# Performance work log

Hardware: AMD Instinct MI355X
Metric: run time of the kernel (lower is better)

The kernel has to match this reference:

```python
import jax, jax.numpy as jnp
import numpy as np

DEP_NUM, HEAD_NUM, BSZ, DIM, REL = 96, 96, 16, 512, 128


def setup_inputs() -> dict:
    key = jax.random.key(0)
    k1, k2, k3, k4 = jax.random.split(key, 4)
    outs = jax.random.normal(k1, (DEP_NUM, BSZ, DIM), dtype=jnp.float32)
    graph_state = jax.random.normal(k2, (HEAD_NUM, BSZ, DIM), dtype=jnp.float32)
    # nn.init.normal_(std=0.02) for both weights, zero biases
    Wt = 0.02 * jax.random.normal(k3, (DIM, 2 * DIM), dtype=jnp.float32)
    bt = jnp.zeros((DIM,), dtype=jnp.float32)
    Wp = 0.02 * jax.random.normal(k4, (REL, DIM), dtype=jnp.float32)
    bp = jnp.zeros((REL,), dtype=jnp.float32)
    return {"outs": outs, "graph_state": graph_state, "Wt": Wt, "bt": bt, "Wp": Wp, "bp": bp}


def reference(outs, graph_state, Wt, bt, Wp, bp):
    # outs: [dep, b, D], graph_state: [head, b, D]
    # Linear(cat(dep, head)) == dep @ Wt[:, :D].T + head @ Wt[:, D:].T + bt
    D = outs.shape[-1]
    dep_proj = jnp.einsum('dbi,ei->dbe', outs, Wt[:, :D])           # [dep, b, D]
    head_proj = jnp.einsum('hbi,ei->hbe', graph_state, Wt[:, D:])   # [head, b, D]
    # broadcast-sum to pairwise: [dep, b, head, D]
    h = jax.nn.relu(dep_proj[:, :, None, :] + jnp.swapaxes(head_proj, 0, 1)[None] + bt)
    # dropout: identity in eval mode
    scores = jnp.einsum('dbhe,re->dbhr', h, Wp) + bp                # [dep, b, head, REL]
    nil = jnp.zeros(scores.shape[:-1] + (1,), dtype=scores.dtype)
    scores = jnp.concatenate([nil, scores], axis=-1)                # [dep, b, head, REL+1]
    return jax.nn.log_softmax(scores, axis=-1)
```

## Files before the change

### kernel.cpp

```cpp
#include <hip/hip_runtime.h>
#include <math.h>

#define DEP   96
#define HEADS 96
#define BSZ   16
#define DIM   512
#define REL   128
#define RELP  129

typedef __attribute__((ext_vector_type(8))) _Float16  half8;
typedef __attribute__((ext_vector_type(2))) __fp16    fp16x2;
typedef __attribute__((ext_vector_type(4))) float     floatx4;

__device__ __forceinline__ unsigned short f2h(float x) {
    union { _Float16 h; unsigned short u; } c;
    c.h = (_Float16)x;
    return c.u;
}
__device__ __forceinline__ unsigned pk_f2h(float a, float b) {
    union { fp16x2 h; unsigned u; } c;
    c.h = __builtin_amdgcn_cvt_pkrtz(a, b);
    return c.u;
}
__device__ __forceinline__ unsigned pk_add_h2(unsigned a, unsigned b) {
    unsigned r; asm("v_pk_add_f16 %0, %1, %2" : "=v"(r) : "v"(a), "v"(b)); return r;
}
__device__ __forceinline__ unsigned pk_max_h2(unsigned a, unsigned b) {
    unsigned r; asm("v_pk_max_f16 %0, %1, %2" : "=v"(r) : "v"(a), "v"(b)); return r;
}

#define PSS 72

__global__ __launch_bounds__(256) void proj_kernel(
    const float* __restrict__ outs, const float* __restrict__ graph,
    const float* __restrict__ Wt, const float* __restrict__ bt,
    const float* __restrict__ Wp,
    float* __restrict__ P1, unsigned short* __restrict__ P2H,
    unsigned short* __restrict__ WpH)
{
    {
        const int fb = (blockIdx.z * gridDim.y + blockIdx.y) * gridDim.x + blockIdx.x;
        if (fb < 32) {
            const int c = fb * 256 + (int)threadIdx.x;
            float4 a = *(const float4*)(Wp + (size_t)c * 8);
            float4 b = *(const float4*)(Wp + (size_t)c * 8 + 4);
            uint4 o;
            o.x = pk_f2h(a.x, a.y); o.y = pk_f2h(a.z, a.w);
            o.z = pk_f2h(b.x, b.y); o.w = pk_f2h(b.z, b.w);
            *(uint4*)(WpH + (size_t)c * 8) = o;
        }
    }

    const int z = blockIdx.z;
    const float* A = z ? graph : outs;
    const int off  = z ? DIM : 0;
    const int row0 = blockIdx.y * 32;
    const int col0 = blockIdx.x * 64;

    __shared__ __align__(16) unsigned short As[32 * PSS];
    __shared__ __align__(16) unsigned short Ws[64 * PSS];

    const int tid  = threadIdx.x;
    const int lane = tid & 63;
    const int wv   = tid >> 6;
    const int ln15 = lane & 15;
    const int quad = lane >> 4;
    const int mh   = wv & 1;
    const int nh   = wv >> 1;

    floatx4 acc[2];
    acc[0] = (floatx4){0.f,0.f,0.f,0.f};
    acc[1] = (floatx4){0.f,0.f,0.f,0.f};

    for (int kt = 0; kt < DIM; kt += 64) {
        {
            const int r  = tid >> 3;
            const int e8 = (tid & 7) * 8;
            const float* p = A + (size_t)(row0 + r) * DIM + kt + e8;
            float4 va = *(const float4*)p;
            float4 vb = *(const float4*)(p + 4);
            uint4 o;
            o.x = pk_f2h(va.x, va.y); o.y = pk_f2h(va.z, va.w);
            o.z = pk_f2h(vb.x, vb.y); o.w = pk_f2h(vb.z, vb.w);
            *(uint4*)&As[r * PSS + e8] = o;
        }
        #pragma unroll
        for (int q = 0; q < 2; ++q) {
            const int slot = q*256 + tid;
            const int r  = slot >> 3;
            const int e8 = (slot & 7) * 8;
            const float* p = Wt + (size_t)(col0 + r) * (2*DIM) + off + kt + e8;
            float4 va = *(const float4*)p;
            float4 vb = *(const float4*)(p + 4);
            uint4 o;
            o.x = pk_f2h(va.x, va.y); o.y = pk_f2h(va.z, va.w);
            o.z = pk_f2h(vb.x, vb.y); o.w = pk_f2h(vb.z, vb.w);
            *(uint4*)&Ws[r * PSS + e8] = o;
        }
        __syncthreads();
        #pragma unroll
        for (int ks = 0; ks < 64; ks += 32) {
            half8 af = *(const half8*)&As[(mh*16 + ln15) * PSS + ks + quad*8];
            #pragma unroll
            for (int nt = 0; nt < 2; ++nt) {
                half8 bf8 = *(const half8*)&Ws[(nh*32 + nt*16 + ln15) * PSS + ks + quad*8];
                acc[nt] = __builtin_amdgcn_mfma_f32_16x16x32_f16(af, bf8, acc[nt], 0, 0, 0);
            }
        }
        __syncthreads();
    }

    #pragma unroll
    for (int nt = 0; nt < 2; ++nt) {
        #pragma unroll
        for (int reg = 0; reg < 4; ++reg) {
            const int m = row0 + mh*16 + quad*4 + reg;
            const int n = col0 + nh*32 + nt*16 + ln15;
            float v = acc[nt][reg];
            if (!z) P1[(size_t)m * DIM + n] = v + bt[n];
            else    P2H[(size_t)m * DIM + n] = f2h(v);
        }
    }
}

#define HSS 72
#define WSS 72

__global__ __launch_bounds__(256, 4) void fused_kernel(
    const float* __restrict__ P1, const unsigned short* __restrict__ P2H,
    const unsigned short* __restrict__ WpH, const float* __restrict__ bp,
    float* __restrict__ out)
{
    const int db = blockIdx.x;
    const int b  = db & 15;

    __shared__ __align__(16) char arena[96*HSS*2 + 128*WSS*2];
    unsigned short* hs = (unsigned short*)arena;
    unsigned short* ws = (unsigned short*)(arena + 96*HSS*2);
    float* outb = (float*)arena;
    float* pmx  = (float*)(arena + 24768);
    float* pl   = pmx + 192;
    float* lseS = pl + 192;

    const int tid  = threadIdx.x;
    const int lane = tid & 63;
    const int wv   = tid >> 6;
    const int ln15 = lane & 15;
    const int quad = lane >> 4;
    const int mh   = wv & 1;
    const int nh   = wv >> 1;
    const int e8   = (tid & 7) * 8;

    const float* drow = P1 + (size_t)db * DIM;

    floatx4 acc[3][4];
    #pragma unroll
    for (int i = 0; i < 3; ++i)
        #pragma unroll
        for (int j = 0; j < 4; ++j) acc[i][j] = (floatx4){0.f,0.f,0.f,0.f};

    for (int kt = 0; kt < DIM; kt += 64) {
        float4 d0 = *(const float4*)(drow + kt + e8);
        float4 d1 = *(const float4*)(drow + kt + e8 + 4);
        uint4 dv;
        dv.x = pk_f2h(d0.x, d0.y); dv.y = pk_f2h(d0.z, d0.w);
        dv.z = pk_f2h(d1.x, d1.y); dv.w = pk_f2h(d1.z, d1.w);

        #pragma unroll
        for (int q = 0; q < 3; ++q) {
            const int h = (q*256 + tid) >> 3;
            uint4 pv = *(const uint4*)(P2H + ((size_t)h * BSZ + b) * DIM + kt + e8);
            uint4 o;
            o.x = pk_max_h2(pk_add_h2(pv.x, dv.x), 0u);
            o.y = pk_max_h2(pk_add_h2(pv.y, dv.y), 0u);
            o.z = pk_max_h2(pk_add_h2(pv.z, dv.z), 0u);
            o.w = pk_max_h2(pk_add_h2(pv.w, dv.w), 0u);
            *(uint4*)&hs[h * HSS + e8] = o;
        }
        #pragma unroll
        for (int q = 0; q < 4; ++q) {
            const int r = (q*256 + tid) >> 3;
            *(uint4*)&ws[r * WSS + e8] =
                *(const uint4*)(WpH + (size_t)r * DIM + kt + e8);
        }
        __syncthreads();

        #pragma unroll
        for (int ks = 0; ks < 64; ks += 32) {
            half8 af[3], bf[4];
            #pragma unroll
            for (int mt = 0; mt < 3; ++mt)
                af[mt] = *(const half8*)&hs[(mh*48 + mt*16 + ln15) * HSS + ks + quad*8];
            #pragma unroll
            for (int nt = 0; nt < 4; ++nt)
                bf[nt] = *(const half8*)&ws[(nh*64 + nt*16 + ln15) * WSS + ks + quad*8];
            #pragma unroll
            for (int nt = 0; nt < 4; ++nt)
                #pragma unroll
                for (int mt = 0; mt < 3; ++mt)
                    acc[mt][nt] = __builtin_amdgcn_mfma_f32_16x16x32_f16(
                        af[mt], bf[nt], acc[mt][nt], 0, 0, 0);
        }
        __syncthreads();
    }

    float bpv[4];
    #pragma unroll
    for (int nt = 0; nt < 4; ++nt) bpv[nt] = bp[nh*64 + nt*16 + ln15];

    #pragma unroll
    for (int mt = 0; mt < 3; ++mt) {
        #pragma unroll
        for (int reg = 0; reg < 4; ++reg) {
            const int m = mh*48 + mt*16 + quad*4 + reg;
            float s[4];
            #pragma unroll
            for (int nt = 0; nt < 4; ++nt) s[nt] = acc[mt][nt][reg] + bpv[nt];
            float mx = fmaxf(fmaxf(s[0], s[1]), fmaxf(s[2], s[3]));
            #pragma unroll
            for (int msk = 1; msk < 16; msk <<= 1) mx = fmaxf(mx, __shfl_xor(mx, msk));
            float l = 0.f;
            #pragma unroll
            for (int nt = 0; nt < 4; ++nt) l += __expf(s[nt] - mx);
            #pragma unroll
            for (int msk = 1; msk < 16; msk <<= 1) l += __shfl_xor(l, msk);
            if (ln15 == 0) { pmx[m*2 + nh] = mx; pl[m*2 + nh] = l; }
        }
    }
    __syncthreads();

    if (tid < 96) {
        const float mx0 = pmx[tid*2], mx1 = pmx[tid*2 + 1];
        const float MX = fmaxf(fmaxf(mx0, mx1), 0.f);
        const float L  = pl[tid*2] * __expf(mx0 - MX) + pl[tid*2 + 1] * __expf(mx1 - MX)
                       + __expf(-MX);
        lseS[tid] = MX + __logf(L);
    }
    __syncthreads();

    #pragma unroll
    for (int g = 0; g < 2; ++g) {
        if (mh == g) {
            #pragma unroll
            for (int mt = 0; mt < 3; ++mt) {
                #pragma unroll
                for (int reg = 0; reg < 4; ++reg) {
                    const int lrow = mt*16 + quad*4 + reg;
                    const float lse = lseS[g*48 + lrow];
                    #pragma unroll
                    for (int nt = 0; nt < 4; ++nt)
                        outb[lrow*RELP + 1 + nh*64 + nt*16 + ln15] =
                            acc[mt][nt][reg] + bpv[nt] - lse;
                    if (nh == 0 && ln15 == 0) outb[lrow*RELP] = -lse;
                }
            }
        }
        __syncthreads();
        float4* gout = (float4*)(out + (size_t)db * (HEADS*RELP) + g * (48*RELP));
        const float4* lsrc = (const float4*)outb;
        for (int j = tid; j < 1548; j += 256)
            gout[j] = lsrc[j];
        __syncthreads();
    }
}

extern "C" void kernel_launch(void* const* d_in, const int* in_sizes, int n_in,
                              void* d_out, int out_size, void* d_ws, size_t ws_size,
                              hipStream_t stream) {
    const float* outs  = (const float*)d_in[0];
    const float* graph = (const float*)d_in[1];
    const float* Wt    = (const float*)d_in[2];
    const float* bt    = (const float*)d_in[3];
    const float* Wp    = (const float*)d_in[4];
    const float* bp    = (const float*)d_in[5];
    float* out = (float*)d_out;

    float* P1           = (float*)d_ws;
    unsigned short* P2H = (unsigned short*)(P1 + 786432);
    unsigned short* WpH = P2H + 786432;

    proj_kernel<<<dim3(DIM/64, (DEP*BSZ)/32, 2), 256, 0, stream>>>(
        outs, graph, Wt, bt, Wp, P1, P2H, WpH);
    fused_kernel<<<DEP*BSZ, 256, 0, stream>>>(P1, P2H, WpH, bp, out);
}
```

Measured before the change: 160.0 us.

## Shrink LDS footprint with 32-wide K tiles and direct output stores

Halves the K tile from 64 to 32, shrinking the shared-memory arena from about 31KB to about 19KB. The dep row is converted to fp16 once into LDS instead of being reloaded from global memory every K step. The LDS-staged coalesced float4 output write is dropped in favour of direct scattered global stores from the MFMA registers. The aim is more resident blocks per CU and fewer redundant loads, at the cost of twice as many barriers in the K loop and less coalesced output writes.

```diff
diff --git a/kernel.cpp b/kernel.cpp
--- a/kernel.cpp
+++ b/kernel.cpp
@@ -123,8 +123,7 @@
     }
 }
 
-#define HSS 72
-#define WSS 72
+#define HS2 40
 
 __global__ __launch_bounds__(256, 4) void fused_kernel(
     const float* __restrict__ P1, const unsigned short* __restrict__ P2H,
@@ -134,11 +133,11 @@
     const int db = blockIdx.x;
     const int b  = db & 15;
 
-    __shared__ __align__(16) char arena[96*HSS*2 + 128*WSS*2];
-    unsigned short* hs = (unsigned short*)arena;
-    unsigned short* ws = (unsigned short*)(arena + 96*HSS*2);
-    float* outb = (float*)arena;
-    float* pmx  = (float*)(arena + 24768);
+    __shared__ __align__(16) char arena[18944];
+    unsigned short* hs    = (unsigned short*)arena;
+    unsigned short* ws    = (unsigned short*)(arena + 7680);
+    unsigned short* drowH = (unsigned short*)(arena + 17920);
+    float* pmx  = (float*)arena;
     float* pl   = pmx + 192;
     float* lseS = pl + 192;
 
@@ -149,9 +148,14 @@
     const int quad = lane >> 4;
     const int mh   = wv & 1;
     const int nh   = wv >> 1;
-    const int e8   = (tid & 7) * 8;
-
-    const float* drow = P1 + (size_t)db * DIM;
+    const int e8   = (tid & 3) * 8;
+    const int r0   = tid >> 2;
+
+    {
+        float2 v = *(const float2*)(P1 + (size_t)db * DIM + tid*2);
+        *(unsigned*)&drowH[tid*2] = pk_f2h(v.x, v.y);
+    }
+    __syncthreads();
 
     floatx4 acc[3][4];
     #pragma unroll
@@ -159,41 +163,44 @@
         #pragma unroll
         for (int j = 0; j < 4; ++j) acc[i][j] = (floatx4){0.f,0.f,0.f,0.f};
 
-    for (int kt = 0; kt < DIM; kt += 64) {
-        float4 d0 = *(const float4*)(drow + kt + e8);
-        float4 d1 = *(const float4*)(drow + kt + e8 + 4);
-        uint4 dv;
-        dv.x = pk_f2h(d0.x, d0.y); dv.y = pk_f2h(d0.z, d0.w);
-        dv.z = pk_f2h(d1.x, d1.y); dv.w = pk_f2h(d1.z, d1.w);
-
-        #pragma unroll
-        for (int q = 0; q < 3; ++q) {
-            const int h = (q*256 + tid) >> 3;
+    for (int kt = 0; kt < DIM; kt += 32) {
+        uint4 dv = *(const uint4*)&drowH[kt + e8];
+        {
+            const int h = r0;
             uint4 pv = *(const uint4*)(P2H + ((size_t)h * BSZ + b) * DIM + kt + e8);
             uint4 o;
             o.x = pk_max_h2(pk_add_h2(pv.x, dv.x), 0u);
             o.y = pk_max_h2(pk_add_h2(pv.y, dv.y), 0u);
             o.z = pk_max_h2(pk_add_h2(pv.z, dv.z), 0u);
             o.w = pk_max_h2(pk_add_h2(pv.w, dv.w), 0u);
-            *(uint4*)&hs[h * HSS + e8] = o;
-        }
-        #pragma unroll
-        for (int q = 0; q < 4; ++q) {
-            const int r = (q*256 + tid) >> 3;
-            *(uint4*)&ws[r * WSS + e8] =
+            *(uint4*)&hs[h * HS2 + e8] = o;
+        }
+        if (tid < 128) {
+            const int h = 64 + r0;
+            uint4 pv = *(const uint4*)(P2H + ((size_t)h * BSZ + b) * DIM + kt + e8);
+            uint4 o;
+            o.x = pk_max_h2(pk_add_h2(pv.x, dv.x), 0u);
+            o.y = pk_max_h2(pk_add_h2(pv.y, dv.y), 0u);
+            o.z = pk_max_h2(pk_add_h2(pv.z, dv.z), 0u);
+            o.w = pk_max_h2(pk_add_h2(pv.w, dv.w), 0u);
+            *(uint4*)&hs[h * HS2 + e8] = o;
+        }
+        #pragma unroll
+        for (int q = 0; q < 2; ++q) {
+            const int r = q*64 + r0;
+            *(uint4*)&ws[r * HS2 + e8] =
                 *(const uint4*)(WpH + (size_t)r * DIM + kt + e8);
         }
         __syncthreads();
 
-        #pragma unroll
-        for (int ks = 0; ks < 64; ks += 32) {
+        {
             half8 af[3], bf[4];
             #pragma unroll
             for (int mt = 0; mt < 3; ++mt)
-                af[mt] = *(const half8*)&hs[(mh*48 + mt*16 + ln15) * HSS + ks + quad*8];
+                af[mt] = *(const half8*)&hs[(mh*48 + mt*16 + ln15) * HS2 + quad*8];
             #pragma unroll
             for (int nt = 0; nt < 4; ++nt)
-                bf[nt] = *(const half8*)&ws[(nh*64 + nt*16 + ln15) * WSS + ks + quad*8];
+                bf[nt] = *(const half8*)&ws[(nh*64 + nt*16 + ln15) * HS2 + quad*8];
             #pragma unroll
             for (int nt = 0; nt < 4; ++nt)
                 #pragma unroll
@@ -239,28 +246,17 @@
     __syncthreads();
 
     #pragma unroll
-    for (int g = 0; g < 2; ++g) {
-        if (mh == g) {
-            #pragma unroll
-            for (int mt = 0; mt < 3; ++mt) {
-                #pragma unroll
-                for (int reg = 0; reg < 4; ++reg) {
-                    const int lrow = mt*16 + quad*4 + reg;
-                    const float lse = lseS[g*48 + lrow];
-                    #pragma unroll
-                    for (int nt = 0; nt < 4; ++nt)
-                        outb[lrow*RELP + 1 + nh*64 + nt*16 + ln15] =
-                            acc[mt][nt][reg] + bpv[nt] - lse;
-                    if (nh == 0 && ln15 == 0) outb[lrow*RELP] = -lse;
-                }
-            }
-        }
-        __syncthreads();
-        float4* gout = (float4*)(out + (size_t)db * (HEADS*RELP) + g * (48*RELP));
-        const float4* lsrc = (const float4*)outb;
-        for (int j = tid; j < 1548; j += 256)
-            gout[j] = lsrc[j];
-        __syncthreads();
+    for (int mt = 0; mt < 3; ++mt) {
+        #pragma unroll
+        for (int reg = 0; reg < 4; ++reg) {
+            const int m = mh*48 + mt*16 + quad*4 + reg;
+            const float lse = lseS[m];
+            const size_t base = ((size_t)db * HEADS + m) * RELP;
+            #pragma unroll
+            for (int nt = 0; nt < 4; ++nt)
+                out[base + 1 + nh*64 + nt*16 + ln15] = acc[mt][nt][reg] + bpv[nt] - lse;
+            if (nh == 0 && ln15 == 0) out[base] = -lse;
+        }
     }
 }
 
```

Result: faster. 151.3 us (-5.5%).
